# Optimization experiments

Measured on AMD Instinct MI355X. Metric: run time of the kernel, lower is better.

The kernel has to match this reference:

```python
import jax, jax.numpy as jnp
import numpy as np

D_MODEL = 512
D_STATE = 64
D_INNER = 2 * D_MODEL   # standard Mamba expand=2
D_CONV = 4
DT_RANK = D_MODEL // 16  # 32
LN_EPS = 1e-5


def setup_inputs() -> dict:
    key = jax.random.key(0)
    ks = jax.random.split(key, 12)
    B, L = 2, 1024
    s = 0.02
    return {
        "frames": jax.random.normal(ks[0], (B, L, D_MODEL), jnp.float32),
        "gamma": jnp.ones((D_MODEL,), jnp.float32),
        "beta": jnp.zeros((D_MODEL,), jnp.float32),
        "W_in": jax.random.normal(ks[1], (D_MODEL, 2 * D_INNER), jnp.float32) * s,
        "conv_w": jax.random.normal(ks[2], (D_INNER, D_CONV), jnp.float32) * s,
        "conv_b": jnp.zeros((D_INNER,), jnp.float32),
        "W_x": jax.random.normal(ks[3], (D_INNER, DT_RANK + 2 * D_STATE), jnp.float32) * s,
        "W_dt": jax.random.normal(ks[4], (DT_RANK, D_INNER), jnp.float32) * s,
        "b_dt": jax.random.uniform(ks[5], (D_INNER,), jnp.float32, -4.0, -2.0),
        "A_log": jnp.log(jnp.broadcast_to(jnp.arange(1, D_STATE + 1, dtype=jnp.float32), (D_INNER, D_STATE))),
        "D": jnp.ones((D_INNER,), jnp.float32),
        "W_out": jax.random.normal(ks[6], (D_INNER, D_MODEL), jnp.float32) * s,
    }


def reference(frames, gamma, beta, W_in, conv_w, conv_b, W_x, W_dt, b_dt, A_log, D, W_out):
    B, L, _ = frames.shape
    d_inner = W_in.shape[1] // 2
    d_state = A_log.shape[1]
    dt_rank = W_dt.shape[0]
    d_conv = conv_w.shape[1]

    # LayerNorm
    mu = frames.mean(-1, keepdims=True)
    var = ((frames - mu) ** 2).mean(-1, keepdims=True)
    xn = (frames - mu) * jax.lax.rsqrt(var + LN_EPS) * gamma + beta

    # in_proj -> x, z
    x, z = jnp.split(xn @ W_in, 2, axis=-1)  # each (B, L, d_inner)

    # causal depthwise conv1d along time
    xc = jnp.pad(x.transpose(0, 2, 1), ((0, 0), (0, 0), (d_conv - 1, 0)))  # (B, d_inner, L+pad)
    xconv = jax.lax.conv_general_dilated(
        xc, conv_w[:, None, :], (1,), "VALID", feature_group_count=d_inner)  # (B, d_inner, L)
    x = jax.nn.silu(xconv.transpose(0, 2, 1) + conv_b)  # (B, L, d_inner)

    # input-dependent dt, B, C
    xdb = x @ W_x
    dt, Bm, Cm = jnp.split(xdb, [dt_rank, dt_rank + d_state], axis=-1)
    delta = jax.nn.softplus(dt @ W_dt + b_dt)  # (B, L, d_inner)
    A = -jnp.exp(A_log)                        # (d_inner, d_state)

    # selective scan over time
    def step(h, inp):
        d_t, B_t, C_t, x_t = inp  # (B,d_inner) (B,d_state) (B,d_state) (B,d_inner)
        dA = jnp.exp(d_t[..., None] * A)                       # (B,d_inner,d_state)
        h = h * dA + (d_t * x_t)[..., None] * B_t[:, None, :]  # (B,d_inner,d_state)
        y = jnp.einsum("bds,bs->bd", h, C_t)
        return h, y

    h0 = jnp.zeros((B, d_inner, d_state), frames.dtype)
    xs = (delta.transpose(1, 0, 2), Bm.transpose(1, 0, 2),
          Cm.transpose(1, 0, 2), x.transpose(1, 0, 2))
    _, ys = jax.lax.scan(step, h0, xs)  # (L, B, d_inner)

    y = ys.transpose(1, 0, 2) + x * D
    y = y * jax.nn.silu(z)
    return y @ W_out + frames  # residual connection
```

## Files before the change

### kernel.cpp

```cpp
#include <hip/hip_runtime.h>
#include <hip/hip_bf16.h>
#include <math.h>

constexpr int Bn     = 2;
constexpr int Lseq   = 1024;
constexpr int DM     = 512;
constexpr int DI     = 1024;
constexpr int DS     = 64;
constexpr int RNK    = 32;
constexpr int NROWS  = Bn * Lseq;
constexpr int XDBW   = RNK + 2 * DS;
constexpr int CH     = 64;
constexpr int NC     = Lseq / CH;

typedef __attribute__((ext_vector_type(4))) float floatx4;
typedef __attribute__((ext_vector_type(8))) short shortx8;

__device__ __forceinline__ float silu_f(float v) {
    return v / (1.f + __expf(-v));
}

__device__ __forceinline__ float rdl(float v, int l) {
    return __int_as_float(__builtin_amdgcn_readlane(__float_as_int(v), l));
}

__global__ void ln_kernel(const float* __restrict__ x, const float* __restrict__ g,
                          const float* __restrict__ be, __hip_bfloat16* __restrict__ xn) {
    int row = blockIdx.x;
    int tid = threadIdx.x;
    const float* xr = x + (size_t)row * DM;
    float v0 = xr[tid], v1 = xr[tid + 256];
    float s = v0 + v1, sq = v0 * v0 + v1 * v1;
    #pragma unroll
    for (int o = 1; o < 64; o <<= 1) {
        s  += __shfl_xor(s, o);
        sq += __shfl_xor(sq, o);
    }
    __shared__ float red[8];
    int w = tid >> 6;
    if ((tid & 63) == 0) { red[w] = s; red[4 + w] = sq; }
    __syncthreads();
    float ts = red[0] + red[1] + red[2] + red[3];
    float tq = red[4] + red[5] + red[6] + red[7];
    float mu  = ts * (1.f / DM);
    float var = tq * (1.f / DM) - mu * mu;
    float inv = rsqrtf(var + 1e-5f);
    __hip_bfloat16* o0 = xn + (size_t)row * DM;
    o0[tid]       = __float2bfloat16((v0 - mu) * inv * g[tid]       + be[tid]);
    o0[tid + 256] = __float2bfloat16((v1 - mu) * inv * g[tid + 256] + be[tid + 256]);
}

__global__ void transpose_cast3(const float* __restrict__ Wi, const float* __restrict__ Wo,
                                const float* __restrict__ Wx,
                                __hip_bfloat16* __restrict__ Ti, __hip_bfloat16* __restrict__ To,
                                __hip_bfloat16* __restrict__ Tx) {
    __shared__ float tile[64][65];
    int bid = blockIdx.x;
    const float* in; __hip_bfloat16* out; int R, Cc, bx, by;
    if (bid < 256)      { in = Wi; out = Ti; R = DM; Cc = 2 * DI; bx = bid & 31;        by = bid >> 5; }
    else if (bid < 384) { int b2 = bid - 256; in = Wo; out = To; R = DI; Cc = DM;   bx = b2 & 7;  by = b2 >> 3; }
    else                { int b2 = bid - 384; in = Wx; out = Tx; R = DI; Cc = XDBW; bx = b2 % 3;  by = b2 / 3; }
    int r0 = by * 64, c0 = bx * 64;
    int tid = threadIdx.x;
    #pragma unroll
    for (int i = tid; i < 4096; i += 256) {
        int r = i >> 6, c = i & 63;
        tile[r][c] = (r0 + r < R && c0 + c < Cc) ? in[(size_t)(r0 + r) * Cc + c0 + c] : 0.f;
    }
    __syncthreads();
    #pragma unroll
    for (int i = tid; i < 4096; i += 256) {
        int c = i >> 6, r = i & 63;
        if (r0 + r < R && c0 + c < Cc)
            out[(size_t)(c0 + c) * R + r0 + r] = __float2bfloat16(tile[r][c]);
    }
}

template<bool RES>
__global__ __launch_bounds__(512) void gemm_bf16_512(const __hip_bfloat16* __restrict__ A,
                                                     const __hip_bfloat16* __restrict__ Bt,
                                                     const float* __restrict__ Res,
                                                     float* __restrict__ C,
                                                     int M, int N, int K) {
    __shared__ __hip_bfloat16 As[128 * 32];
    __shared__ __hip_bfloat16 Bs[128 * 32];
    const int tid  = threadIdx.x;
    const int wave = tid >> 6, lane = tid & 63;
    const int m0 = blockIdx.y * 128, n0 = blockIdx.x * 128;
    const int wm = (wave >> 2) * 64, wn = (wave & 3) * 32;

    floatx4 acc[4][2] = {};

    const int arow16 = lane & 15;
    const int kgrp   = lane >> 4;

    for (int k0 = 0; k0 < K; k0 += 32) {
        {
            int i   = tid;
            int row = i >> 2, seg = i & 3;
            int brow = n0 + row; if (brow >= N) brow = N - 1;
            const __hip_bfloat16* gA = A  + (size_t)(m0 + row) * K + k0 + seg * 8;
            const __hip_bfloat16* gB = Bt + (size_t)brow * K + k0 + seg * 8;
            __hip_bfloat16* lA = As + (size_t)(wave * 64) * 8;
            __hip_bfloat16* lB = Bs + (size_t)(wave * 64) * 8;
            __builtin_amdgcn_global_load_lds(
                (const __attribute__((address_space(1))) void*)gA,
                (__attribute__((address_space(3))) void*)lA, 16, 0, 0);
            __builtin_amdgcn_global_load_lds(
                (const __attribute__((address_space(1))) void*)gB,
                (__attribute__((address_space(3))) void*)lB, 16, 0, 0);
        }
        __syncthreads();

        const shortx8* Asv = (const shortx8*)As;
        const shortx8* Bsv = (const shortx8*)Bs;
        shortx8 a[4], b[2];
        #pragma unroll
        for (int i = 0; i < 4; ++i)
            a[i] = Asv[(wm + i * 16 + arow16) * 4 + kgrp];
        #pragma unroll
        for (int j = 0; j < 2; ++j)
            b[j] = Bsv[(wn + j * 16 + arow16) * 4 + kgrp];
        #pragma unroll
        for (int i = 0; i < 4; ++i)
            #pragma unroll
            for (int j = 0; j < 2; ++j)
                acc[i][j] = __builtin_amdgcn_mfma_f32_16x16x32_bf16(a[i], b[j], acc[i][j], 0, 0, 0);
        __syncthreads();
    }

    const int drow = (lane >> 4) * 4;
    const int dcol = lane & 15;
    #pragma unroll
    for (int i = 0; i < 4; ++i)
        #pragma unroll
        for (int j = 0; j < 2; ++j) {
            int rowb = m0 + wm + i * 16 + drow;
            int col  = n0 + wn + j * 16 + dcol;
            if (col < N) {
                #pragma unroll
                for (int r = 0; r < 4; ++r) {
                    size_t idx = (size_t)(rowb + r) * N + col;
                    float v = acc[i][j][r];
                    if (RES) v += Res[idx];
                    C[idx] = v;
                }
            }
        }
}

template<bool RES>
__global__ __launch_bounds__(512) void gemm64_sk(const __hip_bfloat16* __restrict__ A,
                                                 const __hip_bfloat16* __restrict__ Bt,
                                                 const float* __restrict__ Res,
                                                 float* __restrict__ C,
                                                 int M, int N, int K) {
    __shared__ __hip_bfloat16 As[2][64 * 32];
    __shared__ __hip_bfloat16 Bs[2][64 * 32];
    __shared__ float red[256 * 17];
    const int tid  = threadIdx.x;
    const int wave = tid >> 6, lane = tid & 63;
    const int g = wave >> 2, w2 = wave & 3;
    const int m0 = blockIdx.y * 64, n0 = blockIdx.x * 64;
    const int wm = (w2 >> 1) * 32, wn = (w2 & 1) * 32;

    floatx4 acc[2][2] = {};

    const int arow16 = lane & 15;
    const int kgrp   = lane >> 4;
    const int kbeg   = g * (K / 2);

    for (int kk = 0; kk < K / 2; kk += 32) {
        int k0 = kbeg + kk;
        {
            int i   = w2 * 64 + lane;
            int row = i >> 2, seg = i & 3;
            int brow = n0 + row; if (brow >= N) brow = N - 1;
            const __hip_bfloat16* gA = A  + (size_t)(m0 + row) * K + k0 + seg * 8;
            const __hip_bfloat16* gB = Bt + (size_t)brow * K + k0 + seg * 8;
            __hip_bfloat16* lA = As[g] + (size_t)(w2 * 64) * 8;
            __hip_bfloat16* lB = Bs[g] + (size_t)(w2 * 64) * 8;
            __builtin_amdgcn_global_load_lds(
                (const __attribute__((address_space(1))) void*)gA,
                (__attribute__((address_space(3))) void*)lA, 16, 0, 0);
            __builtin_amdgcn_global_load_lds(
                (const __attribute__((address_space(1))) void*)gB,
                (__attribute__((address_space(3))) void*)lB, 16, 0, 0);
        }
        __syncthreads();

        const shortx8* Asv = (const shortx8*)As[g];
        const shortx8* Bsv = (const shortx8*)Bs[g];
        shortx8 a[2], b[2];
        #pragma unroll
        for (int i = 0; i < 2; ++i)
            a[i] = Asv[(wm + i * 16 + arow16) * 4 + kgrp];
        #pragma unroll
        for (int j = 0; j < 2; ++j)
            b[j] = Bsv[(wn + j * 16 + arow16) * 4 + kgrp];
        #pragma unroll
        for (int i = 0; i < 2; ++i)
            #pragma unroll
            for (int j = 0; j < 2; ++j)
                acc[i][j] = __builtin_amdgcn_mfma_f32_16x16x32_bf16(a[i], b[j], acc[i][j], 0, 0, 0);
        __syncthreads();
    }

    int rbase = (w2 * 64 + lane) * 17;
    if (g == 1) {
        #pragma unroll
        for (int i = 0; i < 2; ++i)
            #pragma unroll
            for (int j = 0; j < 2; ++j)
                *(float4*)&red[rbase + (i * 2 + j) * 4] =
                    make_float4(acc[i][j][0], acc[i][j][1], acc[i][j][2], acc[i][j][3]);
    }
    __syncthreads();
    if (g == 0) {
        const int drow = (lane >> 4) * 4;
        const int dcol = lane & 15;
        #pragma unroll
        for (int i = 0; i < 2; ++i)
            #pragma unroll
            for (int j = 0; j < 2; ++j) {
                float4 part = *(const float4*)&red[rbase + (i * 2 + j) * 4];
                int rowb = m0 + wm + i * 16 + drow;
                int col  = n0 + wn + j * 16 + dcol;
                if (col < N) {
                    #pragma unroll
                    for (int r = 0; r < 4; ++r) {
                        size_t idx = (size_t)(rowb + r) * N + col;
                        float v = acc[i][j][r] + (&part.x)[r];
                        if (RES) v += Res[idx];
                        C[idx] = v;
                    }
                }
            }
    }
}

__global__ void conv_silu(const float* __restrict__ xz, const float* __restrict__ cw,
                          const float* __restrict__ cb, float* __restrict__ xcv,
                          __hip_bfloat16* __restrict__ xcv_bf) {
    int idx = blockIdx.x * 256 + threadIdx.x;
    int d = idx & (DI - 1);
    int bt = idx / DI;
    int t = bt & (Lseq - 1);
    int b = bt / Lseq;
    float acc = cb[d];
    #pragma unroll
    for (int k = 0; k < 4; ++k) {
        int tt = t - 3 + k;
        float xv = (tt >= 0) ? xz[((size_t)(b * Lseq + tt)) * (2 * DI) + d] : 0.f;
        acc += xv * cw[d * 4 + k];
    }
    float v = silu_f(acc);
    xcv[idx] = v;
    xcv_bf[idx] = __float2bfloat16(v);
}

__global__ void delta_kernel(const float* __restrict__ xdb, const float* __restrict__ Wdt,
                             const float* __restrict__ bdt, float* __restrict__ delta) {
    int row = blockIdx.y;
    int d = blockIdx.x * 256 + threadIdx.x;
    __shared__ float dtv[RNK];
    if (threadIdx.x < RNK) dtv[threadIdx.x] = xdb[(size_t)row * XDBW + threadIdx.x];
    __syncthreads();
    float acc = bdt[d];
    #pragma unroll
    for (int r = 0; r < RNK; ++r) acc += dtv[r] * Wdt[(size_t)r * DI + d];
    float sp = (acc > 20.f) ? acc : log1pf(__expf(acc));
    delta[(size_t)row * DI + d] = sp;
}

__global__ __launch_bounds__(512) void scan_chunk1(
        const float* __restrict__ delta, const float* __restrict__ xcv,
        const float* __restrict__ xdb, const float* __restrict__ A_log,
        float* __restrict__ hend, float* __restrict__ dsum) {
    __shared__ float Bsh[64][68];
    __shared__ float dsh[8][64];
    __shared__ float xsh[8][64];

    int blk = blockIdx.x;
    int dg  = blk & (DI / 8 - 1);
    int bc  = blk >> 7;
    int c = bc & (NC - 1), b = bc >> 4;
    int tid = threadIdx.x, w = tid >> 6, lane = tid & 63;
    int d = dg * 8 + w;
    int r0 = b * Lseq + c * CH;

    #pragma unroll
    for (int k = 0; k < 2; ++k) {
        int idx = tid + k * 512;
        int row = idx >> 4, j4 = idx & 15;
        float4 v = *(const float4*)&xdb[(size_t)(r0 + row) * XDBW + RNK + j4 * 4];
        *(float4*)&Bsh[row][j4 * 4] = v;
    }
    {
        int t = tid >> 3, ww = tid & 7;
        dsh[ww][t] = delta[(size_t)(r0 + t) * DI + dg * 8 + ww];
        xsh[ww][t] = xcv[(size_t)(r0 + t) * DI + dg * 8 + ww];
    }
    __syncthreads();

    float a = -__expf(A_log[d * DS + lane]);
    float vd  = dsh[w][lane];
    float vpx = vd * xsh[w][lane];
    float h = 0.f;
    #pragma unroll 16
    for (int t = 0; t < CH; ++t) {
        float dt_ = rdl(vd, t);
        float px  = rdl(vpx, t);
        h = h * __expf(dt_ * a) + px * Bsh[t][lane];
    }
    float S = vd;
    #pragma unroll
    for (int o = 1; o < 64; o <<= 1) S += __shfl_xor(S, o);
    size_t base = ((size_t)bc * DI + d) * 64;
    hend[base + lane] = h;
    if (lane == 0) dsum[(size_t)bc * DI + d] = S;
}

__global__ __launch_bounds__(256) void scan_stitch(
        const float* __restrict__ hend, const float* __restrict__ dsum,
        const float* __restrict__ A_log, float* __restrict__ hstart) {
    int idx = blockIdx.x * 4 + (threadIdx.x >> 6);
    int lane = threadIdx.x & 63;
    int b = idx >> 10, d = idx & (DI - 1);
    float a = -__expf(A_log[d * DS + lane]);
    float h = 0.f;
    #pragma unroll
    for (int c = 0; c < NC; ++c) {
        size_t base = ((size_t)(b * NC + c) * DI + d) * 64;
        hstart[base + lane] = h;
        float he = hend[base + lane];
        float S  = dsum[(size_t)(b * NC + c) * DI + d];
        h = he + __expf(a * S) * h;
    }
}

__global__ __launch_bounds__(512) void scan_chunk2(
        const float* __restrict__ delta, const float* __restrict__ xcv,
        const float* __restrict__ xdb, const float* __restrict__ xz,
        const float* __restrict__ A_log, const float* __restrict__ Dp,
        const float* __restrict__ hstart, __hip_bfloat16* __restrict__ y_row) {
    __shared__ unsigned int BCsh[64][65];
    __shared__ float dsh[8][64];
    __shared__ float xsh[8][64];
    __shared__ float zsh[8][64];
    __shared__ float P[8][8 * 65];

    int blk = blockIdx.x;
    int dg  = blk & (DI / 8 - 1);
    int bc  = blk >> 7;
    int c = bc & (NC - 1), b = bc >> 4;
    int tid = threadIdx.x, w = tid >> 6, lane = tid & 63;
    int d = dg * 8 + w;
    int r0 = b * Lseq + c * CH;

    #pragma unroll
    for (int k = 0; k < 2; ++k) {
        int i = tid + k * 512;
        int t = i >> 4, sg = i & 15;
        const float* rowp = &xdb[(size_t)(r0 + t) * XDBW + RNK];
        float4 bv = *(const float4*)&rowp[sg * 4];
        float4 cv = *(const float4*)&rowp[DS + sg * 4];
        uint4 pk;
        #pragma unroll
        for (int j = 0; j < 4; ++j) {
            unsigned int bb = __float_as_uint((&bv.x)[j]);
            unsigned int cc2 = __float_as_uint((&cv.x)[j]);
            (&pk.x)[j] = (cc2 & 0xFFFF0000u) | (bb >> 16);
        }
        *(uint4*)&BCsh[t][sg * 4] = pk;
    }
    {
        int t = tid >> 3, ww = tid & 7;
        dsh[ww][t] = delta[(size_t)(r0 + t) * DI + dg * 8 + ww];
        xsh[ww][t] = xcv[(size_t)(r0 + t) * DI + dg * 8 + ww];
        zsh[ww][t] = xz[(size_t)(r0 + t) * (2 * DI) + DI + dg * 8 + ww];
    }
    __syncthreads();

    float a  = -__expf(A_log[d * DS + lane]);
    float Dv = Dp[d];
    float vd  = dsh[w][lane];
    float vpx = vd * xsh[w][lane];
    float h = hstart[((size_t)bc * DI + d) * 64 + lane];
    float* Pw = P[w];
    float yreg = 0.f;
    const int tr = lane & 7, q = lane >> 3;

    #pragma unroll
    for (int t8 = 0; t8 < 8; ++t8) {
        #pragma unroll
        for (int tt = 0; tt < 8; ++tt) {
            int t = t8 * 8 + tt;
            unsigned int bcp = BCsh[t][lane];
            float Bt = __uint_as_float(bcp << 16);
            float Ct = __uint_as_float(bcp & 0xFFFF0000u);
            float dt_ = rdl(vd, t);
            float px  = rdl(vpx, t);
            h = h * __expf(dt_ * a) + px * Bt;
            Pw[tt * 65 + lane] = h * Ct;
        }
        float sacc = 0.f;
        #pragma unroll
        for (int j = 0; j < 8; ++j) sacc += Pw[tr * 65 + q * 8 + j];
        sacc += __shfl_xor(sacc, 8);
        sacc += __shfl_xor(sacc, 16);
        sacc += __shfl_xor(sacc, 32);
        if (q == t8) yreg = sacc;
    }

    float yv = (yreg + xsh[w][lane] * Dv) * silu_f(zsh[w][lane]);

    __syncthreads();
    float* T = (float*)P;
    T[lane * 9 + w] = yv;
    __syncthreads();
    {
        int t = tid >> 3, dd = tid & 7;
        float v = T[t * 9 + dd];
        y_row[(size_t)(r0 + t) * DI + dg * 8 + dd] = __float2bfloat16(v);
    }
}

extern "C" void kernel_launch(void* const* d_in, const int* in_sizes, int n_in,
                              void* d_out, int out_size, void* d_ws, size_t ws_size,
                              hipStream_t stream) {
    const float* frames = (const float*)d_in[0];
    const float* gamma  = (const float*)d_in[1];
    const float* beta   = (const float*)d_in[2];
    const float* W_in   = (const float*)d_in[3];
    const float* conv_w = (const float*)d_in[4];
    const float* conv_b = (const float*)d_in[5];
    const float* W_x    = (const float*)d_in[6];
    const float* W_dt   = (const float*)d_in[7];
    const float* b_dt   = (const float*)d_in[8];
    const float* A_log  = (const float*)d_in[9];
    const float* Dp     = (const float*)d_in[10];
    const float* W_out  = (const float*)d_in[11];
    float* out = (float*)d_out;

    char* ws = (char*)d_ws;
    __hip_bfloat16* xn_bf  = (__hip_bfloat16*)ws; ws += (size_t)NROWS * DM * 2;
    __hip_bfloat16* Wt_in  = (__hip_bfloat16*)ws; ws += (size_t)(2 * DI) * DM * 2;
    __hip_bfloat16* Wt_out = (__hip_bfloat16*)ws; ws += (size_t)DM * DI * 2;
    __hip_bfloat16* Wt_x   = (__hip_bfloat16*)ws; ws += (size_t)XDBW * DI * 2;
    __hip_bfloat16* y_row  = (__hip_bfloat16*)ws; ws += (size_t)NROWS * DI * 2;
    __hip_bfloat16* xcv_bf = (__hip_bfloat16*)ws; ws += (size_t)NROWS * DI * 2;
    float* xz     = (float*)ws;  ws += (size_t)NROWS * 2 * DI * 4;
    float* xcv    = (float*)ws;  ws += (size_t)NROWS * DI * 4;
    float* xdb    = (float*)ws;  ws += (size_t)NROWS * XDBW * 4;
    float* delta  = (float*)ws;  ws += (size_t)NROWS * DI * 4;
    float* hend   = (float*)ws;  ws += (size_t)Bn * NC * DI * 64 * 4;
    float* hstart = (float*)ws;  ws += (size_t)Bn * NC * DI * 64 * 4;
    float* dsum   = (float*)ws;  ws += (size_t)Bn * NC * DI * 4;

    transpose_cast3<<<432, 256, 0, stream>>>(W_in, W_out, W_x, Wt_in, Wt_out, Wt_x);

    ln_kernel<<<NROWS, 256, 0, stream>>>(frames, gamma, beta, xn_bf);

    gemm_bf16_512<false><<<dim3(2 * DI / 128, NROWS / 128), 512, 0, stream>>>(
        xn_bf, Wt_in, nullptr, xz, NROWS, 2 * DI, DM);

    conv_silu<<<(NROWS * DI) / 256, 256, 0, stream>>>(xz, conv_w, conv_b, xcv, xcv_bf);

    gemm64_sk<false><<<dim3((XDBW + 63) / 64, NROWS / 64), 512, 0, stream>>>(
        xcv_bf, Wt_x, nullptr, xdb, NROWS, XDBW, DI);

    delta_kernel<<<dim3(DI / 256, NROWS), 256, 0, stream>>>(xdb, W_dt, b_dt, delta);

    scan_chunk1<<<Bn * NC * (DI / 8), 512, 0, stream>>>(delta, xcv, xdb, A_log, hend, dsum);
    scan_stitch<<<Bn * DI / 4, 256, 0, stream>>>(hend, dsum, A_log, hstart);
    scan_chunk2<<<Bn * NC * (DI / 8), 512, 0, stream>>>(delta, xcv, xdb, xz, A_log, Dp, hstart, y_row);

    gemm64_sk<true><<<dim3(DM / 64, NROWS / 64), 512, 0, stream>>>(
        y_row, Wt_out, frames, out, NROWS, DM, DI);
}
```

Baseline: 239.2 us.

## Store in_proj output as bf16 split x/z, tile conv and emit transposed scan inputs

The in_proj GEMM now writes bf16 x and z buffers instead of one fp32 xz buffer. The conv becomes a tiled kernel that stages the time window in shared memory and also precomputes silu(z). It writes time-major transposed bf16 copies of the conv output and gated z, so the scan kernels read them contiguously per channel. This halves intermediate traffic and makes scan loads coalesced, at the cost of bf16 rounding on x and z and extra transposed stores.

Result: no change. 236.3 us (-1.2%).

```diff
diff --git a/kernel.cpp b/kernel.cpp
--- a/kernel.cpp
+++ b/kernel.cpp
@@ -22,6 +22,10 @@
 
 __device__ __forceinline__ float rdl(float v, int l) {
     return __int_as_float(__builtin_amdgcn_readlane(__float_as_int(v), l));
+}
+
+__device__ __forceinline__ float bf2f(unsigned short u) {
+    return __uint_as_float((unsigned)u << 16);
 }
 
 __global__ void ln_kernel(const float* __restrict__ x, const float* __restrict__ g,
@@ -76,12 +80,11 @@
     }
 }
 
-template<bool RES>
-__global__ __launch_bounds__(512) void gemm_bf16_512(const __hip_bfloat16* __restrict__ A,
-                                                     const __hip_bfloat16* __restrict__ Bt,
-                                                     const float* __restrict__ Res,
-                                                     float* __restrict__ C,
-                                                     int M, int N, int K) {
+__global__ __launch_bounds__(512) void gemm_inproj(const __hip_bfloat16* __restrict__ A,
+                                                   const __hip_bfloat16* __restrict__ Bt,
+                                                   __hip_bfloat16* __restrict__ xh,
+                                                   __hip_bfloat16* __restrict__ zh,
+                                                   int M, int N, int K) {
     __shared__ __hip_bfloat16 As[128 * 32];
     __shared__ __hip_bfloat16 Bs[128 * 32];
     const int tid  = threadIdx.x;
@@ -98,9 +101,8 @@
         {
             int i   = tid;
             int row = i >> 2, seg = i & 3;
-            int brow = n0 + row; if (brow >= N) brow = N - 1;
             const __hip_bfloat16* gA = A  + (size_t)(m0 + row) * K + k0 + seg * 8;
-            const __hip_bfloat16* gB = Bt + (size_t)brow * K + k0 + seg * 8;
+            const __hip_bfloat16* gB = Bt + (size_t)(n0 + row) * K + k0 + seg * 8;
             __hip_bfloat16* lA = As + (size_t)(wave * 64) * 8;
             __hip_bfloat16* lB = Bs + (size_t)(wave * 64) * 8;
             __builtin_amdgcn_global_load_lds(
@@ -131,21 +133,18 @@
 
     const int drow = (lane >> 4) * 4;
     const int dcol = lane & 15;
+    const bool isz = (n0 >= DI);
+    __hip_bfloat16* dst = isz ? zh : xh;
+    const int coloff = isz ? DI : 0;
     #pragma unroll
     for (int i = 0; i < 4; ++i)
         #pragma unroll
         for (int j = 0; j < 2; ++j) {
             int rowb = m0 + wm + i * 16 + drow;
-            int col  = n0 + wn + j * 16 + dcol;
-            if (col < N) {
-                #pragma unroll
-                for (int r = 0; r < 4; ++r) {
-                    size_t idx = (size_t)(rowb + r) * N + col;
-                    float v = acc[i][j][r];
-                    if (RES) v += Res[idx];
-                    C[idx] = v;
-                }
-            }
+            int col  = n0 + wn + j * 16 + dcol - coloff;
+            #pragma unroll
+            for (int r = 0; r < 4; ++r)
+                dst[(size_t)(rowb + r) * DI + col] = __float2bfloat16(acc[i][j][r]);
         }
 }
 
@@ -239,24 +238,67 @@
     }
 }
 
-__global__ void conv_silu(const float* __restrict__ xz, const float* __restrict__ cw,
-                          const float* __restrict__ cb, float* __restrict__ xcv,
-                          __hip_bfloat16* __restrict__ xcv_bf) {
-    int idx = blockIdx.x * 256 + threadIdx.x;
-    int d = idx & (DI - 1);
-    int bt = idx / DI;
-    int t = bt & (Lseq - 1);
-    int b = bt / Lseq;
-    float acc = cb[d];
-    #pragma unroll
-    for (int k = 0; k < 4; ++k) {
-        int tt = t - 3 + k;
-        float xv = (tt >= 0) ? xz[((size_t)(b * Lseq + tt)) * (2 * DI) + d] : 0.f;
-        acc += xv * cw[d * 4 + k];
-    }
-    float v = silu_f(acc);
-    xcv[idx] = v;
-    xcv_bf[idx] = __float2bfloat16(v);
+__global__ __launch_bounds__(256) void conv_tile(const __hip_bfloat16* __restrict__ xh,
+                                                 const __hip_bfloat16* __restrict__ zh,
+                                                 const float* __restrict__ cw,
+                                                 const float* __restrict__ cb,
+                                                 __hip_bfloat16* __restrict__ xcv_bf,
+                                                 __hip_bfloat16* __restrict__ xcvT,
+                                                 __hip_bfloat16* __restrict__ zgT) {
+    __shared__ float xt[67][68];
+    __shared__ float tb[64][65];
+    __shared__ float tb2[64][65];
+    int t0 = blockIdx.x * 64, d0 = blockIdx.y * 64, b = blockIdx.z;
+    int tid = threadIdx.x;
+    size_t rowbase = (size_t)b * Lseq;
+
+    for (int i = tid; i < 67 * 16; i += 256) {
+        int r = i >> 4, j = i & 15;
+        int t = t0 - 3 + r;
+        float4 v4 = make_float4(0.f, 0.f, 0.f, 0.f);
+        if (t >= 0) {
+            ushort4 u = *(const ushort4*)&xh[(rowbase + t) * DI + d0 + j * 4];
+            v4 = make_float4(bf2f(u.x), bf2f(u.y), bf2f(u.z), bf2f(u.w));
+        }
+        *(float4*)&xt[r][j * 4] = v4;
+    }
+    for (int i = tid; i < 64 * 16; i += 256) {
+        int r = i >> 4, j = i & 15;
+        ushort4 u = *(const ushort4*)&zh[(rowbase + t0 + r) * DI + d0 + j * 4];
+        tb2[r][j * 4 + 0] = silu_f(bf2f(u.x));
+        tb2[r][j * 4 + 1] = silu_f(bf2f(u.y));
+        tb2[r][j * 4 + 2] = silu_f(bf2f(u.z));
+        tb2[r][j * 4 + 3] = silu_f(bf2f(u.w));
+    }
+    __syncthreads();
+
+    {
+        int d = tid & 63, tg = tid >> 6;
+        float4 cwv = *(const float4*)&cw[(d0 + d) * 4];
+        float cbv = cb[d0 + d];
+        #pragma unroll
+        for (int i = 0; i < 16; ++i) {
+            int t = tg * 16 + i;
+            float acc = cbv;
+            #pragma unroll
+            for (int k = 0; k < 4; ++k) acc += xt[t + k][d] * (&cwv.x)[k];
+            float v = silu_f(acc);
+            tb[t][d] = v;
+            xcv_bf[(rowbase + t0 + t) * DI + d0 + d] = __float2bfloat16(v);
+        }
+    }
+    __syncthreads();
+
+    {
+        int t2 = tid & 63, dg2 = tid >> 6;
+        #pragma unroll
+        for (int i = 0; i < 16; ++i) {
+            int d = dg2 * 16 + i;
+            size_t orow = ((size_t)(b * DI + d0 + d)) * Lseq + t0 + t2;
+            xcvT[orow] = __float2bfloat16(tb[t2][d]);
+            zgT[orow]  = __float2bfloat16(tb2[t2][d]);
+        }
+    }
 }
 
 __global__ void delta_kernel(const float* __restrict__ xdb, const float* __restrict__ Wdt,
@@ -274,7 +316,7 @@
 }
 
 __global__ __launch_bounds__(512) void scan_chunk1(
-        const float* __restrict__ delta, const float* __restrict__ xcv,
+        const float* __restrict__ delta, const __hip_bfloat16* __restrict__ xcvT,
         const float* __restrict__ xdb, const float* __restrict__ A_log,
         float* __restrict__ hend, float* __restrict__ dsum) {
     __shared__ float Bsh[64][68];
@@ -299,7 +341,7 @@
     {
         int t = tid >> 3, ww = tid & 7;
         dsh[ww][t] = delta[(size_t)(r0 + t) * DI + dg * 8 + ww];
-        xsh[ww][t] = xcv[(size_t)(r0 + t) * DI + dg * 8 + ww];
+        xsh[w][lane] = bf2f(((const unsigned short*)xcvT)[((size_t)(b * DI + d)) * Lseq + c * CH + lane]);
     }
     __syncthreads();
 
@@ -340,8 +382,8 @@
 }
 
 __global__ __launch_bounds__(512) void scan_chunk2(
-        const float* __restrict__ delta, const float* __restrict__ xcv,
-        const float* __restrict__ xdb, const float* __restrict__ xz,
+        const float* __restrict__ delta, const __hip_bfloat16* __restrict__ xcvT,
+        const float* __restrict__ xdb, const __hip_bfloat16* __restrict__ zgT,
         const float* __restrict__ A_log, const float* __restrict__ Dp,
         const float* __restrict__ hstart, __hip_bfloat16* __restrict__ y_row) {
     __shared__ unsigned int BCsh[64][65];
@@ -377,8 +419,9 @@
     {
         int t = tid >> 3, ww = tid & 7;
         dsh[ww][t] = delta[(size_t)(r0 + t) * DI + dg * 8 + ww];
-        xsh[ww][t] = xcv[(size_t)(r0 + t) * DI + dg * 8 + ww];
-        zsh[ww][t] = xz[(size_t)(r0 + t) * (2 * DI) + DI + dg * 8 + ww];
+        size_t trow = ((size_t)(b * DI + d)) * Lseq + c * CH + lane;
+        xsh[w][lane] = bf2f(((const unsigned short*)xcvT)[trow]);
+        zsh[w][lane] = bf2f(((const unsigned short*)zgT)[trow]);
     }
     __syncthreads();
 
@@ -413,7 +456,7 @@
         if (q == t8) yreg = sacc;
     }
 
-    float yv = (yreg + xsh[w][lane] * Dv) * silu_f(zsh[w][lane]);
+    float yv = (yreg + xsh[w][lane] * Dv) * zsh[w][lane];
 
     __syncthreads();
     float* T = (float*)P;
@@ -450,8 +493,10 @@
     __hip_bfloat16* Wt_x   = (__hip_bfloat16*)ws; ws += (size_t)XDBW * DI * 2;
     __hip_bfloat16* y_row  = (__hip_bfloat16*)ws; ws += (size_t)NROWS * DI * 2;
     __hip_bfloat16* xcv_bf = (__hip_bfloat16*)ws; ws += (size_t)NROWS * DI * 2;
-    float* xz     = (float*)ws;  ws += (size_t)NROWS * 2 * DI * 4;
-    float* xcv    = (float*)ws;  ws += (size_t)NROWS * DI * 4;
+    __hip_bfloat16* xh     = (__hip_bfloat16*)ws; ws += (size_t)NROWS * DI * 2;
+    __hip_bfloat16* zh     = (__hip_bfloat16*)ws; ws += (size_t)NROWS * DI * 2;
+    __hip_bfloat16* xcvT   = (__hip_bfloat16*)ws; ws += (size_t)NROWS * DI * 2;
+    __hip_bfloat16* zgT    = (__hip_bfloat16*)ws; ws += (size_t)NROWS * DI * 2;
     float* xdb    = (float*)ws;  ws += (size_t)NROWS * XDBW * 4;
     float* delta  = (float*)ws;  ws += (size_t)NROWS * DI * 4;
     float* hend   = (float*)ws;  ws += (size_t)Bn * NC * DI * 64 * 4;
@@ -462,19 +507,20 @@
 
     ln_kernel<<<NROWS, 256, 0, stream>>>(frames, gamma, beta, xn_bf);
 
-    gemm_bf16_512<false><<<dim3(2 * DI / 128, NROWS / 128), 512, 0, stream>>>(
-        xn_bf, Wt_in, nullptr, xz, NROWS, 2 * DI, DM);
-
-    conv_silu<<<(NROWS * DI) / 256, 256, 0, stream>>>(xz, conv_w, conv_b, xcv, xcv_bf);
+    gemm_inproj<<<dim3(2 * DI / 128, NROWS / 128), 512, 0, stream>>>(
+        xn_bf, Wt_in, xh, zh, NROWS, 2 * DI, DM);
+
+    conv_tile<<<dim3(Lseq / 64, DI / 64, Bn), 256, 0, stream>>>(
+        xh, zh, conv_w, conv_b, xcv_bf, xcvT, zgT);
 
     gemm64_sk<false><<<dim3((XDBW + 63) / 64, NROWS / 64), 512, 0, stream>>>(
         xcv_bf, Wt_x, nullptr, xdb, NROWS, XDBW, DI);
 
     delta_kernel<<<dim3(DI / 256, NROWS), 256, 0, stream>>>(xdb, W_dt, b_dt, delta);
 
-    scan_chunk1<<<Bn * NC * (DI / 8), 512, 0, stream>>>(delta, xcv, xdb, A_log, hend, dsum);
+    scan_chunk1<<<Bn * NC * (DI / 8), 512, 0, stream>>>(delta, xcvT, xdb, A_log, hend, dsum);
     scan_stitch<<<Bn * DI / 4, 256, 0, stream>>>(hend, dsum, A_log, hstart);
-    scan_chunk2<<<Bn * NC * (DI / 8), 512, 0, stream>>>(delta, xcv, xdb, xz, A_log, Dp, hstart, y_row);
+    scan_chunk2<<<Bn * NC * (DI / 8), 512, 0, stream>>>(delta, xcvT, xdb, zgT, A_log, Dp, hstart, y_row);
 
     gemm64_sk<true><<<dim3(DM / 64, NROWS / 64), 512, 0, stream>>>(
         y_row, Wt_out, frames, out, NROWS, DM, DI);
```
